# Optimization experiments

Hardware: AMD Instinct MI355X
Metric: run time of the kernel (lower is better)

## Reference

```python
import jax, jax.numpy as jnp
import numpy as np

EMBED_DIM = 1024
NUM_HEADS = 16
HEAD_DIM = EMBED_DIM // NUM_HEADS


def setup_inputs() -> dict:
    key = jax.random.key(0)
    ks = jax.random.split(key, 9)
    B, S, D = 2, 2048, EMBED_DIM
    scale = 1.0 / np.sqrt(D)
    x = jax.random.normal(ks[0], (B, S, D), dtype=jnp.float32)
    wq = jax.random.normal(ks[1], (D, D), dtype=jnp.float32) * scale
    bq = jax.random.normal(ks[2], (D,), dtype=jnp.float32) * 0.02
    wk = jax.random.normal(ks[3], (D, D), dtype=jnp.float32) * scale
    bk = jax.random.normal(ks[4], (D,), dtype=jnp.float32) * 0.02
    wv = jax.random.normal(ks[5], (D, D), dtype=jnp.float32) * scale
    bv = jax.random.normal(ks[6], (D,), dtype=jnp.float32) * 0.02
    wo = jax.random.normal(ks[7], (D, D), dtype=jnp.float32) * scale
    bo = jax.random.normal(ks[8], (D,), dtype=jnp.float32) * 0.02
    return {"x": x, "wq": wq, "bq": bq, "wk": wk, "bk": bk,
            "wv": wv, "bv": bv, "wo": wo, "bo": bo}


def reference(x, wq, bq, wk, bk, wv, bv, wo, bo):
    B, S, D = x.shape
    H, Hd = NUM_HEADS, HEAD_DIM
    # separate QKV linears (weights stored [in, out] so x @ w)
    q = (x @ wq + bq).reshape(B, S, H, Hd).transpose(0, 2, 1, 3)  # [B,H,S,Hd]
    k = (x @ wk + bk).reshape(B, S, H, Hd).transpose(0, 2, 1, 3)
    v = (x @ wv + bv).reshape(B, S, H, Hd).transpose(0, 2, 1, 3)
    scores = jnp.einsum('bhqd,bhkd->bhqk', q, k) / jnp.sqrt(jnp.float32(Hd))
    attn = jax.nn.softmax(scores, axis=-1)
    context = jnp.einsum('bhqk,bhkd->bhqd', attn, v)
    context = context.transpose(0, 2, 1, 3).reshape(B, S, D)
    return context @ wo + bo
```

## Files before the change

### kernel.cpp

```cpp
#include <hip/hip_runtime.h>
#include <cstdint>
#include <cstddef>


typedef float floatx4 __attribute__((ext_vector_type(4)));
typedef __bf16 bf16x8 __attribute__((ext_vector_type(8)));
union ABFrag { bf16x8 v; uint4 q; unsigned short u[8]; unsigned int w[4]; };

__device__ __forceinline__ unsigned short f2bf(float f) {
    unsigned int u = __builtin_bit_cast(unsigned int, f);
    return (unsigned short)((u + 0x7FFFu + ((u >> 16) & 1u)) >> 16);
}

__device__ __forceinline__ unsigned int cvtpk(float lo, float hi) {
    unsigned int r;
    asm("v_cvt_pk_bf16_f32 %0, %1, %2" : "=v"(r) : "v"(lo), "v"(hi));
    return r;
}

#if __has_builtin(__builtin_amdgcn_exp2f)
#define EXP2F(x) __builtin_amdgcn_exp2f(x)
#else
#define EXP2F(x) exp2f(x)
#endif

__device__ __forceinline__ void glds16(const void* g, void* l) {
    __builtin_amdgcn_global_load_lds(
        (const __attribute__((address_space(1))) unsigned int*)(uintptr_t)g,
        (__attribute__((address_space(3))) unsigned int*)(unsigned int)(uintptr_t)l,
        16, 0, 0);
}

__global__ void convert_fused_kernel(const float* __restrict__ x,
                                     const float* __restrict__ w0,
                                     const float* __restrict__ w1,
                                     const float* __restrict__ w2,
                                     const float* __restrict__ w3,
                                     unsigned short* __restrict__ xb,
                                     unsigned short* __restrict__ wT) {
    const int tid = threadIdx.x;
    if (blockIdx.x < 2048) {
        int i = (blockIdx.x * 256 + tid) * 8;
        float4 a = *(const float4*)(x + i);
        float4 b = *(const float4*)(x + i + 4);
        union { unsigned short u[8]; uint4 q; } o;
        o.u[0] = f2bf(a.x); o.u[1] = f2bf(a.y); o.u[2] = f2bf(a.z); o.u[3] = f2bf(a.w);
        o.u[4] = f2bf(b.x); o.u[5] = f2bf(b.y); o.u[6] = f2bf(b.z); o.u[7] = f2bf(b.w);
        *(uint4*)(xb + i) = o.q;
        return;
    }
    __shared__ unsigned short t[32][40];
    const int wi = blockIdx.x - 2048;
    const int z  = wi >> 10;
    const int rem = wi & 1023;
    const int k0 = (rem >> 5) * 32, n0 = (rem & 31) * 32;
    const float* w = (z == 0) ? w0 : (z == 1) ? w1 : (z == 2) ? w2 : w3;
    unsigned short* dst = wT + (size_t)z * 1024 * 1024;
    {
        int ry = tid >> 3, cx = (tid & 7) * 4;
        float4 v = *(const float4*)(w + (size_t)(k0 + ry) * 1024 + n0 + cx);
        t[cx + 0][ry] = f2bf(v.x); t[cx + 1][ry] = f2bf(v.y);
        t[cx + 2][ry] = f2bf(v.z); t[cx + 3][ry] = f2bf(v.w);
    }
    __syncthreads();
    int n = tid >> 3, kc = (tid & 7) * 4;
    *(uint2*)(dst + (size_t)(n0 + n) * 1024 + k0 + kc) = *(const uint2*)&t[n][kc];
}

template<int KIND>
__launch_bounds__(256, 2)
__global__ void gemm_kernel(const unsigned short* __restrict__ A,
                            const unsigned short* __restrict__ wT,
                            const float* __restrict__ bias0,
                            const float* __restrict__ bias1,
                            const float* __restrict__ bias2,
                            void* __restrict__ out0,
                            void* __restrict__ out1,
                            void* __restrict__ out2)
{
    constexpr int BM = (KIND == 1) ? 64 : 128;
    constexpr int BN = (KIND == 1) ? 64 : 128;
    constexpr int NI = BM / 32;
    constexpr int NJ = BN / 32;

    __shared__ unsigned short a_s[BM * 32];
    __shared__ unsigned short b_s[BN * 32];

    int bx, by, bz;
    if constexpr (KIND == 0) {
        int lin = blockIdx.x + (blockIdx.y << 3) + (blockIdx.z << 8);
        int swz = (lin & 7) * 96 + (lin >> 3);
        bx = swz & 7;
        int rem = swz >> 3;
        by = rem & 31;
        bz = rem >> 5;
    } else {
        int lin = blockIdx.x + (blockIdx.y << 4);
        int swz = ((lin & 7) << 7) + (lin >> 3);
        bx = swz & 15;
        by = swz >> 4;
        bz = 0;
    }

    const int tid  = threadIdx.x;
    const int wid  = tid >> 6;
    const int lane = tid & 63;
    const int quad = lane >> 4;
    const int l15  = lane & 15;
    const int wm   = (wid >> 1) * (BM / 2);
    const int wn   = (wid & 1) * (BN / 2);
    const int m0   = by * BM;
    const int n0   = bx * BN;

    const unsigned short* Bt = (KIND == 0) ? wT + (size_t)bz * (1024 * 1024) : wT;
    const float* bias = (KIND == 0)
        ? (bz == 0 ? bias0 : bz == 1 ? bias1 : bias2) : bias0;

    const int sr = lane >> 2;
    const int sc = (lane & 3) * 8;
    const unsigned short* gA = A + (size_t)(m0 + wid * (BM / 4) + sr) * 1024 + sc;
    const unsigned short* gB = Bt + (size_t)(n0 + wid * (BN / 4) + sr) * 1024 + sc;
    unsigned short* lA = a_s + wid * (BM / 4) * 32;
    unsigned short* lB = b_s + wid * (BN / 4) * 32;

    floatx4 acc[NI][NJ];
    #pragma unroll
    for (int i = 0; i < NI; i++)
        #pragma unroll
        for (int j = 0; j < NJ; j++)
            acc[i][j] = floatx4{0.f, 0.f, 0.f, 0.f};

    for (int k0 = 0; k0 < 1024; k0 += 32) {
        __syncthreads();
        glds16(gA + k0, lA);
        if constexpr (KIND == 0) glds16(gA + k0 + 16 * 1024, lA + 512);
        glds16(gB + k0, lB);
        if constexpr (KIND == 0) glds16(gB + k0 + 16 * 1024, lB + 512);
        __syncthreads();

        ABFrag af[NI], bf4[NJ];
        #pragma unroll
        for (int i = 0; i < NI; i++)
            af[i].q = *(const uint4*)(a_s + (wm + i * 16 + l15) * 32 + quad * 8);
        #pragma unroll
        for (int j = 0; j < NJ; j++)
            bf4[j].q = *(const uint4*)(b_s + (wn + j * 16 + l15) * 32 + quad * 8);
        #pragma unroll
        for (int i = 0; i < NI; i++)
            #pragma unroll
            for (int j = 0; j < NJ; j++)
                acc[i][j] = __builtin_amdgcn_mfma_f32_16x16x32_bf16(
                    af[i].v, bf4[j].v, acc[i][j], 0, 0, 0);
    }

    if constexpr (KIND == 1) {
        float* out = (float*)out0;
        #pragma unroll
        for (int j = 0; j < NJ; j++) {
            int gn = n0 + wn + j * 16 + l15;
            float bval = bias[gn];
            #pragma unroll
            for (int i = 0; i < NI; i++)
                #pragma unroll
                for (int r = 0; r < 4; r++) {
                    int gm = m0 + wm + i * 16 + quad * 4 + r;
                    out[(size_t)gm * 1024 + gn] = acc[i][j][r] + bval;
                }
        }
    } else {
        if (bz == 0) {
            const float SCQ = 0.125f * 1.44269504088896f;
            unsigned short* out = (unsigned short*)out0;
            #pragma unroll
            for (int j = 0; j < 4; j++) {
                int gn = n0 + wn + j * 16 + l15;
                float bval = bias[gn];
                int h = gn >> 6, d = gn & 63;
                #pragma unroll
                for (int i = 0; i < 4; i++)
                    #pragma unroll
                    for (int r = 0; r < 4; r++) {
                        int gm = m0 + wm + i * 16 + quad * 4 + r;
                        int b = gm >> 11, s = gm & 2047;
                        out[(((size_t)(b * 16 + h) * 2048 + s) << 6) + d] =
                            f2bf((acc[i][j][r] + bval) * SCQ);
                    }
            }
        } else if (bz == 1) {
            unsigned short* out = (unsigned short*)out1;
            #pragma unroll
            for (int j = 0; j < 4; j++) {
                int gn = n0 + wn + j * 16 + l15;
                float bval = bias[gn];
                int h = gn >> 6, d = gn & 63;
                int dg = d >> 3, dl = d & 7;
                #pragma unroll
                for (int i = 0; i < 4; i++)
                    #pragma unroll
                    for (int r = 0; r < 4; r++) {
                        int gm = m0 + wm + i * 16 + quad * 4 + r;
                        int b = gm >> 11, s = gm & 2047;
                        int dphys = ((dg ^ (s & 7)) << 3) | dl;
                        out[(((size_t)(b * 16 + h) * 2048 + s) << 6) + dphys] =
                            f2bf(acc[i][j][r] + bval);
                    }
            }
        } else {
            __shared__ unsigned short t_s[128][136];
            #pragma unroll
            for (int j = 0; j < 4; j++) {
                int nl = wn + j * 16 + l15;
                float bval = bias[n0 + nl];
                #pragma unroll
                for (int i = 0; i < 4; i++)
                    #pragma unroll
                    for (int r = 0; r < 4; r++)
                        t_s[nl][wm + i * 16 + quad * 4 + r] = f2bf(acc[i][j][r] + bval);
            }
            __syncthreads();
            unsigned short* out = (unsigned short*)out2;
            const int n  = tid >> 1, half = tid & 1;
            const int bh = (m0 >> 11) * 16 + ((n0 + n) >> 6);
            const int d  = (n0 + n) & 63;
            const int chunk = ((m0 & 2047) >> 6) + half;
            const int dmask = d & 7;
            unsigned short* dstb = out + ((size_t)(bh * 32 + chunk) * 64 + d) * 64;
            const unsigned short* src = &t_s[n][half * 64];
            #pragma unroll
            for (int gp = 0; gp < 8; gp++) {
                int u1 = 32 * (gp >> 2) + 4 * (gp & 3);
                uint2 lo = *(const uint2*)(src + u1);
                uint2 hi = *(const uint2*)(src + u1 + 16);
                unsigned short* dq = dstb + ((gp ^ dmask) << 3);
                *(uint2*)dq       = lo;
                *(uint2*)(dq + 4) = hi;
            }
        }
    }
}

__launch_bounds__(512, 4)
__global__ void attn_kernel(const unsigned short* __restrict__ Q,
                            const unsigned short* __restrict__ K,
                            const unsigned short* __restrict__ Vt,
                            unsigned short* __restrict__ ctx)
{
    __shared__ unsigned short smem[2][2][2][4096];

    const int lin = blockIdx.x + (blockIdx.y << 4);
    const int swz = ((lin & 7) << 6) + (lin >> 3);
    const int qx  = swz & 15;
    const int bh  = swz >> 4;

    const int tid  = threadIdx.x;
    const int wid  = tid >> 6;
    const int kh   = wid >> 2;
    const int wq   = wid & 3;
    const int lane = tid & 63;
    const int quad = lane >> 4;
    const int l15  = lane & 15;
    const int xr   = l15 & 7;

    const unsigned short* Qh = Q + (size_t)bh * (2048 * 64);
    const char* Kc = (const char*)(K  + (size_t)bh * (2048 * 64)) + (size_t)kh * (16 * 8192);
    const char* Vc = (const char*)(Vt + (size_t)bh * (2048 * 64)) + (size_t)kh * (16 * 8192);
    const int q0 = qx * 128 + wq * 32;

    ABFrag qf[2][2];
    #pragma unroll
    for (int jq = 0; jq < 2; jq++)
        #pragma unroll
        for (int s = 0; s < 2; s++)
            qf[jq][s].q = *(const uint4*)(Qh + (size_t)(q0 + jq * 16 + l15) * 64
                                          + s * 32 + quad * 8);

    int kcol[2];
    kcol[0] = ((quad    ) ^ xr) << 3;
    kcol[1] = ((quad + 4) ^ xr) << 3;

    floatx4 acc[4][2];
    #pragma unroll
    for (int i = 0; i < 4; i++)
        #pragma unroll
        for (int jq = 0; jq < 2; jq++)
            acc[i][jq] = floatx4{0.f, 0.f, 0.f, 0.f};
    float lrun[2] = {0.f, 0.f};

    auto stage = [&](int c, int b) {
        const char* gk = Kc + (size_t)c * 8192 + wq * 2048 + lane * 16;
        char* lk = (char*)&smem[b][kh][0][0] + wq * 2048;
        glds16(gk,        lk);
        glds16(gk + 1024, lk + 1024);
        const char* gv = Vc + (size_t)c * 8192 + wq * 2048 + lane * 16;
        char* lv = (char*)&smem[b][kh][1][0] + wq * 2048;
        glds16(gv,        lv);
        glds16(gv + 1024, lv + 1024);
    };

    stage(0, 0);

    for (int c = 0; c < 16; ++c) {
        const int b = c & 1;
        __syncthreads();
        if (c + 1 < 16) stage(c + 1, b ^ 1);

        const unsigned short* ks = &smem[b][kh][0][0];
        const unsigned short* vs = &smem[b][kh][1][0];

        floatx4 st[4][2];
        #pragma unroll
        for (int kt = 0; kt < 4; kt++) {
            ABFrag k0, k1;
            const unsigned short* kr = ks + (kt * 16 + l15) * 64;
            k0.q = *(const uint4*)(kr + kcol[0]);
            k1.q = *(const uint4*)(kr + kcol[1]);
            #pragma unroll
            for (int jq = 0; jq < 2; jq++) {
                floatx4 t = floatx4{0.f, 0.f, 0.f, 0.f};
                t = __builtin_amdgcn_mfma_f32_16x16x32_bf16(k0.v, qf[jq][0].v, t, 0, 0, 0);
                t = __builtin_amdgcn_mfma_f32_16x16x32_bf16(k1.v, qf[jq][1].v, t, 0, 0, 0);
                st[kt][jq] = t;
            }
        }

        unsigned int pk[4][2][2];
        #pragma unroll
        for (int jq = 0; jq < 2; jq++) {
            float ls = 0.f;
            #pragma unroll
            for (int kt = 0; kt < 4; kt++) {
                #pragma unroll
                for (int t2 = 0; t2 < 2; t2++) {
                    float p0 = EXP2F(st[kt][jq][2 * t2 + 0]);
                    float p1 = EXP2F(st[kt][jq][2 * t2 + 1]);
                    ls += p0 + p1;
                    pk[kt][jq][t2] = cvtpk(p0, p1);
                }
            }
            lrun[jq] += ls;
        }

        #pragma unroll
        for (int s2 = 0; s2 < 2; s2++) {
            ABFrag pf[2];
            #pragma unroll
            for (int jq = 0; jq < 2; jq++) {
                pf[jq].w[0] = pk[2 * s2 + 0][jq][0];
                pf[jq].w[1] = pk[2 * s2 + 0][jq][1];
                pf[jq].w[2] = pk[2 * s2 + 1][jq][0];
                pf[jq].w[3] = pk[2 * s2 + 1][jq][1];
            }
            #pragma unroll
            for (int i = 0; i < 4; i++) {
                ABFrag vf;
                vf.q = *(const uint4*)(vs + (i * 16 + l15) * 64 + kcol[s2]);
                #pragma unroll
                for (int jq = 0; jq < 2; jq++)
                    acc[i][jq] = __builtin_amdgcn_mfma_f32_16x16x32_bf16(
                        vf.v, pf[jq].v, acc[i][jq], 0, 0, 0);
            }
        }
    }

    __syncthreads();
    float* sf = (float*)&smem[0][0][0][0];
    float* myp = sf + (size_t)(wq * 64 + lane) * 40;
    if (kh) {
        #pragma unroll
        for (int i = 0; i < 4; i++)
            #pragma unroll
            for (int jq = 0; jq < 2; jq++)
                *(floatx4*)(myp + (i * 2 + jq) * 4) = acc[i][jq];
        myp[32] = lrun[0];
        myp[33] = lrun[1];
    }
    __syncthreads();
    if (!kh) {
        #pragma unroll
        for (int i = 0; i < 4; i++)
            #pragma unroll
            for (int jq = 0; jq < 2; jq++)
                acc[i][jq] += *(const floatx4*)(myp + (i * 2 + jq) * 4);
        lrun[0] += myp[32];
        lrun[1] += myp[33];

        const int b_ = bh >> 4, h = bh & 15;
        #pragma unroll
        for (int jq = 0; jq < 2; jq++) {
            float s = lrun[jq];
            s += __shfl_xor(s, 16, 64);
            s += __shfl_xor(s, 32, 64);
            float inv = 1.0f / s;
            int q = q0 + jq * 16 + l15;
            size_t base = (size_t)(b_ * 2048 + q) * 1024 + h * 64;
            #pragma unroll
            for (int i = 0; i < 4; i++) {
                float v0 = acc[i][jq][0] * inv, v1 = acc[i][jq][1] * inv;
                float v2 = acc[i][jq][2] * inv, v3 = acc[i][jq][3] * inv;
                uint2 w2 = make_uint2(cvtpk(v0, v1), cvtpk(v2, v3));
                *(uint2*)(ctx + base + i * 16 + quad * 4) = w2;
            }
        }
    }
}

extern "C" void kernel_launch(void* const* d_in, const int* in_sizes, int n_in,
                              void* d_out, int out_size, void* d_ws, size_t ws_size,
                              hipStream_t stream)
{
    const float* x  = (const float*)d_in[0];
    const float* wq = (const float*)d_in[1];
    const float* bq = (const float*)d_in[2];
    const float* wk = (const float*)d_in[3];
    const float* bk = (const float*)d_in[4];
    const float* wv = (const float*)d_in[5];
    const float* bv = (const float*)d_in[6];
    const float* wo = (const float*)d_in[7];
    const float* bo = (const float*)d_in[8];

    const size_t NE = (size_t)4096 * 1024;
    unsigned short* xb  = (unsigned short*)d_ws;
    unsigned short* wT  = xb  + NE;
    unsigned short* qb  = wT  + NE;
    unsigned short* kb  = qb  + NE;
    unsigned short* vtb = kb  + NE;
    unsigned short* ctx = vtb + NE;

    hipLaunchKernelGGL(convert_fused_kernel, dim3(6144), dim3(256), 0, stream,
                       x, wq, wk, wv, wo, xb, wT);
    hipLaunchKernelGGL((gemm_kernel<0>), dim3(8, 32, 3), dim3(256), 0, stream,
                       xb, wT, bq, bk, bv, (void*)qb, (void*)kb, (void*)vtb);
    hipLaunchKernelGGL(attn_kernel, dim3(16, 32), dim3(512), 0, stream, qb, kb, vtb, ctx);
    hipLaunchKernelGGL((gemm_kernel<1>), dim3(16, 64), dim3(256), 0, stream,
                       ctx, wT + 3 * NE / 4, bo, nullptr, nullptr, d_out, nullptr, nullptr);
}
```

Baseline: 184.5 us.

## Double per-warp query tile in attention kernel to 64 rows

Each attention block now covers 256 queries instead of 128, and each wave handles four 16-row query tiles instead of two. Every K/V fragment read from shared memory therefore feeds twice as many MFMAs, which halves K/V loads per query and halves the block count. The cross-half partial reduction is split into two passes through shared memory so it still fits in the existing buffer. In exchange, register pressure roughly doubles (launch bounds lowered to 2 blocks), and the grid shrinks to 256 blocks, which reduces occupancy and latency hiding.

```diff
diff --git a/kernel.cpp b/kernel.cpp
--- a/kernel.cpp
+++ b/kernel.cpp
@@ -172,12 +172,12 @@
             const float SCQ = 0.125f * 1.44269504088896f;
             unsigned short* out = (unsigned short*)out0;
             #pragma unroll
-            for (int j = 0; j < 4; j++) {
+            for (int j = 0; j < NJ; j++) {
                 int gn = n0 + wn + j * 16 + l15;
                 float bval = bias[gn];
                 int h = gn >> 6, d = gn & 63;
                 #pragma unroll
-                for (int i = 0; i < 4; i++)
+                for (int i = 0; i < NI; i++)
                     #pragma unroll
                     for (int r = 0; r < 4; r++) {
                         int gm = m0 + wm + i * 16 + quad * 4 + r;
@@ -189,13 +189,13 @@
         } else if (bz == 1) {
             unsigned short* out = (unsigned short*)out1;
             #pragma unroll
-            for (int j = 0; j < 4; j++) {
+            for (int j = 0; j < NJ; j++) {
                 int gn = n0 + wn + j * 16 + l15;
                 float bval = bias[gn];
                 int h = gn >> 6, d = gn & 63;
                 int dg = d >> 3, dl = d & 7;
                 #pragma unroll
-                for (int i = 0; i < 4; i++)
+                for (int i = 0; i < NI; i++)
                     #pragma unroll
                     for (int r = 0; r < 4; r++) {
                         int gm = m0 + wm + i * 16 + quad * 4 + r;
@@ -208,11 +208,11 @@
         } else {
             __shared__ unsigned short t_s[128][136];
             #pragma unroll
-            for (int j = 0; j < 4; j++) {
+            for (int j = 0; j < NJ; j++) {
                 int nl = wn + j * 16 + l15;
                 float bval = bias[n0 + nl];
                 #pragma unroll
-                for (int i = 0; i < 4; i++)
+                for (int i = 0; i < NI; i++)
                     #pragma unroll
                     for (int r = 0; r < 4; r++)
                         t_s[nl][wm + i * 16 + quad * 4 + r] = f2bf(acc[i][j][r] + bval);
@@ -239,7 +239,7 @@
     }
 }
 
-__launch_bounds__(512, 4)
+__launch_bounds__(512, 2)
 __global__ void attn_kernel(const unsigned short* __restrict__ Q,
                             const unsigned short* __restrict__ K,
                             const unsigned short* __restrict__ Vt,
@@ -247,10 +247,10 @@
 {
     __shared__ unsigned short smem[2][2][2][4096];
 
-    const int lin = blockIdx.x + (blockIdx.y << 4);
-    const int swz = ((lin & 7) << 6) + (lin >> 3);
-    const int qx  = swz & 15;
-    const int bh  = swz >> 4;
+    const int lin = blockIdx.x + (blockIdx.y << 3);
+    const int swz = ((lin & 7) << 5) + (lin >> 3);
+    const int qx  = swz & 7;
+    const int bh  = swz >> 3;
 
     const int tid  = threadIdx.x;
     const int wid  = tid >> 6;
@@ -264,11 +264,11 @@
     const unsigned short* Qh = Q + (size_t)bh * (2048 * 64);
     const char* Kc = (const char*)(K  + (size_t)bh * (2048 * 64)) + (size_t)kh * (16 * 8192);
     const char* Vc = (const char*)(Vt + (size_t)bh * (2048 * 64)) + (size_t)kh * (16 * 8192);
-    const int q0 = qx * 128 + wq * 32;
-
-    ABFrag qf[2][2];
+    const int q0 = qx * 256 + wq * 64;
+
+    ABFrag qf[4][2];
     #pragma unroll
-    for (int jq = 0; jq < 2; jq++)
+    for (int jq = 0; jq < 4; jq++)
         #pragma unroll
         for (int s = 0; s < 2; s++)
             qf[jq][s].q = *(const uint4*)(Qh + (size_t)(q0 + jq * 16 + l15) * 64
@@ -278,13 +278,13 @@
     kcol[0] = ((quad    ) ^ xr) << 3;
     kcol[1] = ((quad + 4) ^ xr) << 3;
 
-    floatx4 acc[4][2];
+    floatx4 acc[4][4];
     #pragma unroll
     for (int i = 0; i < 4; i++)
         #pragma unroll
-        for (int jq = 0; jq < 2; jq++)
+        for (int jq = 0; jq < 4; jq++)
             acc[i][jq] = floatx4{0.f, 0.f, 0.f, 0.f};
-    float lrun[2] = {0.f, 0.f};
+    float lrun[4] = {0.f, 0.f, 0.f, 0.f};
 
     auto stage = [&](int c, int b) {
         const char* gk = Kc + (size_t)c * 8192 + wq * 2048 + lane * 16;
@@ -307,7 +307,7 @@
         const unsigned short* ks = &smem[b][kh][0][0];
         const unsigned short* vs = &smem[b][kh][1][0];
 
-        floatx4 st[4][2];
+        floatx4 st[4][4];
         #pragma unroll
         for (int kt = 0; kt < 4; kt++) {
             ABFrag k0, k1;
@@ -315,7 +315,7 @@
             k0.q = *(const uint4*)(kr + kcol[0]);
             k1.q = *(const uint4*)(kr + kcol[1]);
             #pragma unroll
-            for (int jq = 0; jq < 2; jq++) {
+            for (int jq = 0; jq < 4; jq++) {
                 floatx4 t = floatx4{0.f, 0.f, 0.f, 0.f};
                 t = __builtin_amdgcn_mfma_f32_16x16x32_bf16(k0.v, qf[jq][0].v, t, 0, 0, 0);
                 t = __builtin_amdgcn_mfma_f32_16x16x32_bf16(k1.v, qf[jq][1].v, t, 0, 0, 0);
@@ -323,9 +323,9 @@
             }
         }
 
-        unsigned int pk[4][2][2];
-        #pragma unroll
-        for (int jq = 0; jq < 2; jq++) {
+        unsigned int pk[4][4][2];
+        #pragma unroll
+        for (int jq = 0; jq < 4; jq++) {
             float ls = 0.f;
             #pragma unroll
             for (int kt = 0; kt < 4; kt++) {
@@ -342,9 +342,9 @@
 
         #pragma unroll
         for (int s2 = 0; s2 < 2; s2++) {
-            ABFrag pf[2];
-            #pragma unroll
-            for (int jq = 0; jq < 2; jq++) {
+            ABFrag pf[4];
+            #pragma unroll
+            for (int jq = 0; jq < 4; jq++) {
                 pf[jq].w[0] = pk[2 * s2 + 0][jq][0];
                 pf[jq].w[1] = pk[2 * s2 + 0][jq][1];
                 pf[jq].w[2] = pk[2 * s2 + 1][jq][0];
@@ -355,7 +355,7 @@
                 ABFrag vf;
                 vf.q = *(const uint4*)(vs + (i * 16 + l15) * 64 + kcol[s2]);
                 #pragma unroll
-                for (int jq = 0; jq < 2; jq++)
+                for (int jq = 0; jq < 4; jq++)
                     acc[i][jq] = __builtin_amdgcn_mfma_f32_16x16x32_bf16(
                         vf.v, pf[jq].v, acc[i][jq], 0, 0, 0);
             }
@@ -364,29 +364,49 @@
 
     __syncthreads();
     float* sf = (float*)&smem[0][0][0][0];
-    float* myp = sf + (size_t)(wq * 64 + lane) * 40;
+    float* myp = sf + (size_t)(wq * 64 + lane) * 36;
     if (kh) {
         #pragma unroll
-        for (int i = 0; i < 4; i++)
-            #pragma unroll
-            for (int jq = 0; jq < 2; jq++)
-                *(floatx4*)(myp + (i * 2 + jq) * 4) = acc[i][jq];
+        for (int i = 0; i < 2; i++)
+            #pragma unroll
+            for (int jq = 0; jq < 4; jq++)
+                *(floatx4*)(myp + (i * 4 + jq) * 4) = acc[i][jq];
         myp[32] = lrun[0];
         myp[33] = lrun[1];
     }
     __syncthreads();
     if (!kh) {
         #pragma unroll
-        for (int i = 0; i < 4; i++)
-            #pragma unroll
-            for (int jq = 0; jq < 2; jq++)
-                acc[i][jq] += *(const floatx4*)(myp + (i * 2 + jq) * 4);
+        for (int i = 0; i < 2; i++)
+            #pragma unroll
+            for (int jq = 0; jq < 4; jq++)
+                acc[i][jq] += *(const floatx4*)(myp + (i * 4 + jq) * 4);
         lrun[0] += myp[32];
         lrun[1] += myp[33];
+    }
+    __syncthreads();
+    if (kh) {
+        #pragma unroll
+        for (int i = 2; i < 4; i++)
+            #pragma unroll
+            for (int jq = 0; jq < 4; jq++)
+                *(floatx4*)(myp + ((i - 2) * 4 + jq) * 4) = acc[i][jq];
+        myp[32] = lrun[2];
+        myp[33] = lrun[3];
+    }
+    __syncthreads();
+    if (!kh) {
+        #pragma unroll
+        for (int i = 2; i < 4; i++)
+            #pragma unroll
+            for (int jq = 0; jq < 4; jq++)
+                acc[i][jq] += *(const floatx4*)(myp + ((i - 2) * 4 + jq) * 4);
+        lrun[2] += myp[32];
+        lrun[3] += myp[33];
 
         const int b_ = bh >> 4, h = bh & 15;
         #pragma unroll
-        for (int jq = 0; jq < 2; jq++) {
+        for (int jq = 0; jq < 4; jq++) {
             float s = lrun[jq];
             s += __shfl_xor(s, 16, 64);
             s += __shfl_xor(s, 32, 64);
@@ -430,7 +450,7 @@
                        x, wq, wk, wv, wo, xb, wT);
     hipLaunchKernelGGL((gemm_kernel<0>), dim3(8, 32, 3), dim3(256), 0, stream,
                        xb, wT, bq, bk, bv, (void*)qb, (void*)kb, (void*)vtb);
-    hipLaunchKernelGGL(attn_kernel, dim3(16, 32), dim3(512), 0, stream, qb, kb, vtb, ctx);
+    hipLaunchKernelGGL(attn_kernel, dim3(8, 32), dim3(512), 0, stream, qb, kb, vtb, ctx);
     hipLaunchKernelGGL((gemm_kernel<1>), dim3(16, 64), dim3(256), 0, stream,
                        ctx, wT + 3 * NE / 4, bo, nullptr, nullptr, d_out, nullptr, nullptr);
 }
```

Measured after the change: 180.1 us, median of 3. 2.4% less time.
